# Kernel tuning notes

Hardware: AMD Instinct MI355X
Metric: run time of the kernel (lower is better)

The kernel has to match this reference:

```python
import jax, jax.numpy as jnp
import numpy as np

EPS = 1e-7  # keras backend epsilon

def setup_inputs() -> dict:
    key = jax.random.key(0)
    k1, k2, k3 = jax.random.split(key, 3)
    B, L, D, P = 16, 1024, 256, 20
    sent1 = jax.random.normal(k1, (B, L, D), dtype=jnp.float32)
    sent2 = jax.random.normal(k2, (B, L, D), dtype=jnp.float32)
    kernel = jax.random.normal(k3, (P, D), dtype=jnp.float32) * 0.1
    return {"sent1": sent1, "sent2": sent2, "kernel": kernel}

def reference(sent1, sent2, kernel):
    # token norms with keras-style clamping: sqrt(max(sum(x^2), eps))
    n1 = jnp.sqrt(jnp.maximum(jnp.sum(sent1 * sent1, axis=-1), EPS))  # [B,L1]
    n2 = jnp.sqrt(jnp.maximum(jnp.sum(sent2 * sent2, axis=-1), EPS))  # [B,L2]
    # all-pairs cosine matrix via matmul instead of broadcast-multiply-reduce
    dots = jnp.einsum('bld,bmd->blm', sent1, sent2)                    # [B,L1,L2]
    cos = dots / n1[:, :, None] / n2[:, None, :]
    # mean attentive vectors: cosine-weighted sum of sent2, normalized by row sum
    weighted = jnp.einsum('blm,bmd->bld', cos, sent2)                  # [B,L1,D]
    mav = weighted / (jnp.sum(cos, axis=-1, keepdims=True) + EPS)      # [B,L1,D]
    # perspective-weighted cosine between sent1*k and mav*k, fused without [B,L,P,D]
    k2 = kernel * kernel                                               # [P,D]
    num = jnp.einsum('bld,pd->blp', sent1 * mav, k2)                   # sum_d s1*mav*k^2
    nv1 = jnp.sqrt(jnp.maximum(jnp.einsum('bld,pd->blp', sent1 * sent1, k2), EPS))
    nv2 = jnp.sqrt(jnp.maximum(jnp.einsum('bld,pd->blp', mav * mav, k2), EPS))
    return num / nv1 / nv2                                             # [B,L1,P]
```

## Files before the change

kernel.cpp:

```cpp
#include <hip/hip_runtime.h>
#include <math.h>

#define EPS 1e-7f

constexpr int B = 16, L = 1024, D = 256, P = 20;
constexpr int LD = L * D;
constexpr int DD = D * D;

typedef __attribute__((ext_vector_type(8))) _Float16 f16x8;
typedef __attribute__((ext_vector_type(4))) float f32x4;


__device__ inline unsigned short f2h(float x) {
    _Float16 h = (_Float16)x;
    union { _Float16 h; unsigned short u; } c; c.h = h; return c.u;
}
__device__ inline float h2f(unsigned short u) {
    union { unsigned short u; _Float16 h; } c; c.u = u; return (float)c.h;
}

__global__ __launch_bounds__(256) void k_prep2(const float* __restrict__ s2,
                                               float* __restrict__ tp,
                                               unsigned short* __restrict__ CT) {
    __shared__ float tile[32][257];
    __shared__ float wiv[32];
    __shared__ float wsq[32];
    int tid = threadIdx.x;
    int b   = blockIdx.x >> 5, mt = blockIdx.x & 31;
    int m0  = mt * 32;
    {
        int r = tid >> 3, c0 = (tid & 7) * 32;
        const float* gp = s2 + (size_t)b * LD + (size_t)(m0 + r) * D + c0;
        float4 v[8];
#pragma unroll
        for (int q = 0; q < 8; ++q) v[q] = ((const float4*)gp)[q];
#pragma unroll
        for (int q = 0; q < 8; ++q) *(float4*)&tile[r][c0 + q * 4] = v[q];
    }
    __syncthreads();
    {
        int r = tid >> 3, seg = tid & 7;
        float s = 0.f;
#pragma unroll
        for (int k = 0; k < 32; ++k) { float v = tile[r][seg * 32 + k]; s += v * v; }
#pragma unroll
        for (int o = 4; o; o >>= 1) s += __shfl_down(s, o, 8);
        if (seg == 0) {
            float iv = 1.0f / sqrtf(fmaxf(s, EPS));
            wiv[r] = iv;
            wsq[r] = sqrtf(iv);
        }
    }
    __syncthreads();
    {
        int dc = tid;
        float tpart = 0.f;
        union { unsigned short us[32]; uint4 q[4]; } ph;
#pragma unroll
        for (int m = 0; m < 32; ++m) {
            float v = tile[m][dc];
            tpart += v * wiv[m];
            ph.us[m] = f2h(v * wsq[m]);
        }
        tp[(size_t)(mt * B + b) * D + dc] = tpart;
        size_t o = (size_t)b * LD + (size_t)dc * L + m0;
        *(uint4*)(CT + o)      = ph.q[0]; *(uint4*)(CT + o + 8)  = ph.q[1];
        *(uint4*)(CT + o + 16) = ph.q[2]; *(uint4*)(CT + o + 24) = ph.q[3];
    }
}

__global__ __launch_bounds__(256) void k_gram32(const unsigned short* __restrict__ CT,
                                                unsigned short* __restrict__ Gf) {
    __shared__ short smem[2 * 32 * 264];
    short* As = smem;
    short* Bs = smem + 32 * 264;
    int tid  = threadIdx.x;
    int b    = blockIdx.x >> 6;
    int ti   = (blockIdx.x >> 3) & 7;
    int tj   = blockIdx.x & 7;
    int wave = tid >> 6, lane = tid & 63;
    int lr   = lane & 15, lq = lane >> 4;
    int srow = tid >> 3, sseg = (tid & 7) * 32;

    f32x4 acc[2][2];
#pragma unroll
    for (int i = 0; i < 2; ++i)
#pragma unroll
        for (int j = 0; j < 2; ++j) acc[i][j] = (f32x4){0.f, 0.f, 0.f, 0.f};

#pragma unroll 1
    for (int kb = 0; kb < 4; ++kb) {
        int koff = kb * 256;
        __syncthreads();
        {
            const unsigned short* ga = CT + (size_t)b * LD + (size_t)(ti * 32 + srow) * L + koff + sseg;
            uint4 a0 = ((const uint4*)ga)[0], a1 = ((const uint4*)ga)[1];
            uint4 a2 = ((const uint4*)ga)[2], a3 = ((const uint4*)ga)[3];
            const unsigned short* gb = CT + (size_t)b * LD + (size_t)(tj * 32 + srow) * L + koff + sseg;
            uint4 b0 = ((const uint4*)gb)[0], b1 = ((const uint4*)gb)[1];
            uint4 b2 = ((const uint4*)gb)[2], b3 = ((const uint4*)gb)[3];
            short* la = &As[srow * 264 + sseg];
            ((uint4*)la)[0] = a0; ((uint4*)la)[1] = a1;
            ((uint4*)la)[2] = a2; ((uint4*)la)[3] = a3;
            short* lb = &Bs[srow * 264 + sseg];
            ((uint4*)lb)[0] = b0; ((uint4*)lb)[1] = b1;
            ((uint4*)lb)[2] = b2; ((uint4*)lb)[3] = b3;
        }
        __syncthreads();
#pragma unroll
        for (int kk = 0; kk < 2; ++kk) {
            int ks = wave * 2 + kk;
            f16x8 af[2], bf[2];
#pragma unroll
            for (int i = 0; i < 2; ++i)
                af[i] = *(const f16x8*)&As[(i * 16 + lr) * 264 + ks * 32 + lq * 8];
#pragma unroll
            for (int j = 0; j < 2; ++j)
                bf[j] = *(const f16x8*)&Bs[(j * 16 + lr) * 264 + ks * 32 + lq * 8];
#pragma unroll
            for (int i = 0; i < 2; ++i)
#pragma unroll
                for (int j = 0; j < 2; ++j)
                    acc[i][j] = __builtin_amdgcn_mfma_f32_16x16x32_f16(af[i], bf[j], acc[i][j], 0, 0, 0);
        }
    }
    __syncthreads();
    float* red = (float*)smem;
#pragma unroll
    for (int i = 0; i < 2; ++i)
#pragma unroll
        for (int j = 0; j < 2; ++j)
#pragma unroll
            for (int r = 0; r < 4; ++r) {
                int row = i * 16 + lq * 4 + r, col = j * 16 + lr;
                red[wave * 1056 + row * 33 + col] = acc[i][j][r];
            }
    __syncthreads();
#pragma unroll
    for (int k = 0; k < 4; ++k) {
        int e = tid + k * 256;
        int row = e >> 5, col = e & 31;
        float s = red[row * 33 + col] + red[1056 + row * 33 + col] +
                  red[2112 + row * 33 + col] + red[3168 + row * 33 + col];
        Gf[(size_t)b * DD + (size_t)(ti * 32 + row) * D + tj * 32 + col] = f2h(s);
    }
}

__global__ __launch_bounds__(512) void k_mav_out(const float* __restrict__ s1,
                                                 const float* __restrict__ tp,
                                                 const unsigned short* __restrict__ Gf,
                                                 const float* __restrict__ kern,
                                                 float* __restrict__ out) {
    __shared__ short As[32 * 264];
    __shared__ short Bs[64 * 264];
    __shared__ short Ms[32 * 264];
    __shared__ float ts[D];
    __shared__ float sgnS[32];
    int tid  = threadIdx.x;
    int b    = blockIdx.x >> 5, lt = blockIdx.x & 31;
    int l0   = lt * 32;
    int wave = tid >> 6, lane = tid & 63;
    int lr   = lane & 15, lq = lane >> 4;

    if (tid < 256) {
        float a = 0.f;
#pragma unroll
        for (int mc = 0; mc < 32; ++mc) a += tp[(size_t)(mc * B + b) * D + tid];
        ts[tid] = a;
    }
    __syncthreads();

    {
        int r = tid >> 4, seg = tid & 15;
        const float* gp = s1 + (size_t)(b * L + l0 + r) * D + seg * 16;
        float up = 0.f, sq = 0.f;
        union { unsigned short us[16]; uint4 q[2]; } hb;
#pragma unroll
        for (int q4 = 0; q4 < 4; ++q4) {
            float4 v = ((const float4*)gp)[q4];
            int td = seg * 16 + q4 * 4;
            up += v.x * ts[td] + v.y * ts[td + 1] + v.z * ts[td + 2] + v.w * ts[td + 3];
            sq += v.x * v.x + v.y * v.y + v.z * v.z + v.w * v.w;
            hb.us[q4 * 4 + 0] = f2h(v.x); hb.us[q4 * 4 + 1] = f2h(v.y);
            hb.us[q4 * 4 + 2] = f2h(v.z); hb.us[q4 * 4 + 3] = f2h(v.w);
        }
        short* la = &As[r * 264 + seg * 16];
        ((uint4*)la)[0] = hb.q[0]; ((uint4*)la)[1] = hb.q[1];
#pragma unroll
        for (int o = 8; o; o >>= 1) { up += __shfl_down(up, o, 16); sq += __shfl_down(sq, o, 16); }
        if (seg == 0) {
            float n1v = sqrtf(fmaxf(sq, EPS));
            sgnS[r] = up + EPS * n1v;
        }
    }

    int wlr = (wave >> 2) * 16;
    int wnc = (wave & 3) * 16;
#pragma unroll 1
    for (int nh = 0; nh < 4; ++nh) {
        __syncthreads();
        {
            int r = tid >> 3, seg = (tid & 7) * 32;
            const unsigned short* gb = Gf + (size_t)b * DD + (size_t)(nh * 64 + r) * D + seg;
            uint4 b0 = ((const uint4*)gb)[0], b1 = ((const uint4*)gb)[1];
            uint4 b2 = ((const uint4*)gb)[2], b3 = ((const uint4*)gb)[3];
            short* lb = &Bs[r * 264 + seg];
            ((uint4*)lb)[0] = b0; ((uint4*)lb)[1] = b1;
            ((uint4*)lb)[2] = b2; ((uint4*)lb)[3] = b3;
        }
        __syncthreads();
        f32x4 acc = (f32x4){0.f, 0.f, 0.f, 0.f};
#pragma unroll
        for (int ks = 0; ks < 8; ++ks) {
            f16x8 af = *(const f16x8*)&As[(wlr + lr) * 264 + ks * 32 + lq * 8];
            f16x8 bf = *(const f16x8*)&Bs[(wnc + lr) * 264 + ks * 32 + lq * 8];
            acc = __builtin_amdgcn_mfma_f32_16x16x32_f16(af, bf, acc, 0, 0, 0);
        }
#pragma unroll
        for (int r4 = 0; r4 < 4; ++r4)
            Ms[(wlr + lq * 4 + r4) * 264 + nh * 64 + wnc + lr] = f2h(acc[r4]);
    }
    __syncthreads();

    float* k2s = (float*)Bs;
    {
        int d = tid & 255, ph = tid >> 8;
#pragma unroll
        for (int i = 0; i < 10; ++i) {
            int p = i * 2 + ph;
            float v = kern[p * D + d];
            k2s[p * 264 + d] = v * v;
        }
    }
    __syncthreads();

    int dg = lane & 15, ps = lane >> 4;
#pragma unroll 1
    for (int rl = 0; rl < 4; ++rl) {
        int l = wave * 4 + rl;
        float4 sm[4], ss[4], mm[4];
#pragma unroll
        for (int j = 0; j < 4; ++j) {
            ushort4 h4 = *(const ushort4*)&As[l * 264 + dg * 4 + j * 64];
            ushort4 m4 = *(const ushort4*)&Ms[l * 264 + dg * 4 + j * 64];
            float4 sv, mv;
            sv.x = h2f(h4.x); sv.y = h2f(h4.y); sv.z = h2f(h4.z); sv.w = h2f(h4.w);
            mv.x = h2f(m4.x); mv.y = h2f(m4.y); mv.z = h2f(m4.z); mv.w = h2f(m4.w);
            sm[j].x = sv.x * mv.x; sm[j].y = sv.y * mv.y; sm[j].z = sv.z * mv.z; sm[j].w = sv.w * mv.w;
            ss[j].x = sv.x * sv.x; ss[j].y = sv.y * sv.y; ss[j].z = sv.z * sv.z; ss[j].w = sv.w * sv.w;
            mm[j].x = mv.x * mv.x; mm[j].y = mv.y * mv.y; mm[j].z = mv.z * mv.z; mm[j].w = mv.w * mv.w;
        }
        float sgn = (sgnS[l] < 0.f) ? -1.f : 1.f;
#pragma unroll
        for (int tI = 0; tI < 5; ++tI) {
            int p = ps + tI * 4;
            float na = 0.f, nb = 0.f, nc = 0.f;
#pragma unroll
            for (int j = 0; j < 4; ++j) {
                float4 kv = *(const float4*)&k2s[p * 264 + j * 64 + dg * 4];
                na += sm[j].x * kv.x + sm[j].y * kv.y + sm[j].z * kv.z + sm[j].w * kv.w;
                nb += ss[j].x * kv.x + ss[j].y * kv.y + ss[j].z * kv.z + ss[j].w * kv.w;
                nc += mm[j].x * kv.x + mm[j].y * kv.y + mm[j].z * kv.z + mm[j].w * kv.w;
            }
#pragma unroll
            for (int o = 8; o; o >>= 1) {
                na += __shfl_down(na, o, 16);
                nb += __shfl_down(nb, o, 16);
                nc += __shfl_down(nc, o, 16);
            }
            if (dg == 0) {
                out[(size_t)(b * L + l0 + l) * P + p] =
                    sgn * na * rsqrtf(fmaxf(nb, EPS)) * rsqrtf(fmaxf(nc, EPS));
            }
        }
    }
}

extern "C" void kernel_launch(void* const* d_in, const int* in_sizes, int n_in,
                              void* d_out, int out_size, void* d_ws, size_t ws_size,
                              hipStream_t stream) {
    const float* s1   = (const float*)d_in[0];
    const float* s2   = (const float*)d_in[1];
    const float* kern = (const float*)d_in[2];
    float* out = (float*)d_out;
    float* ws  = (float*)d_ws;

    float* tp = ws;
    unsigned short* CT = (unsigned short*)(ws + 131072);
    unsigned short* Gf = (unsigned short*)(ws + 2228224);

    k_prep2<<<512, 256, 0, stream>>>(s2, tp, CT);
    k_gram32<<<1024, 256, 0, stream>>>(CT, Gf);
    k_mav_out<<<512, 512, 0, stream>>>(s1, tp, Gf, kern, out);
}
```

Baseline: 126.3 us.

## Load MFMA operands directly from global memory and widen prep kernel to 512 threads

The gram kernel no longer stages CT tiles through LDS. Each wave streams its own K-slice of f16 fragments straight from global memory into MFMA, which removes the per-iteration barriers and LDS copies. The mav kernel likewise reads Gf fragments directly from global memory, keeps its A fragments in registers, and computes the squared kernel up front alongside the ts reduction. The prep kernel doubles its thread count and splits the M dimension across two halves, combining the partial sums through shared memory. This trades LDS reuse for uncoalesced, per-lane 16-byte global loads that depend on cache hits.

Result: slower. 134.1 us (+6.2%).

```diff
diff --git a/kernel.cpp b/kernel.cpp
--- a/kernel.cpp
+++ b/kernel.cpp
@@ -19,32 +19,33 @@
     union { unsigned short u; _Float16 h; } c; c.u = u; return (float)c.h;
 }
 
-__global__ __launch_bounds__(256) void k_prep2(const float* __restrict__ s2,
+__global__ __launch_bounds__(512) void k_prep2(const float* __restrict__ s2,
                                                float* __restrict__ tp,
                                                unsigned short* __restrict__ CT) {
     __shared__ float tile[32][257];
     __shared__ float wiv[32];
     __shared__ float wsq[32];
+    __shared__ float tpp[2][256];
     int tid = threadIdx.x;
     int b   = blockIdx.x >> 5, mt = blockIdx.x & 31;
     int m0  = mt * 32;
     {
-        int r = tid >> 3, c0 = (tid & 7) * 32;
+        int r = tid >> 4, c0 = (tid & 15) * 16;
         const float* gp = s2 + (size_t)b * LD + (size_t)(m0 + r) * D + c0;
-        float4 v[8];
-#pragma unroll
-        for (int q = 0; q < 8; ++q) v[q] = ((const float4*)gp)[q];
-#pragma unroll
-        for (int q = 0; q < 8; ++q) *(float4*)&tile[r][c0 + q * 4] = v[q];
-    }
-    __syncthreads();
-    {
-        int r = tid >> 3, seg = tid & 7;
+        float4 v[4];
+#pragma unroll
+        for (int q = 0; q < 4; ++q) v[q] = ((const float4*)gp)[q];
+#pragma unroll
+        for (int q = 0; q < 4; ++q) *(float4*)&tile[r][c0 + q * 4] = v[q];
+    }
+    __syncthreads();
+    {
+        int r = tid >> 4, seg = tid & 15;
         float s = 0.f;
 #pragma unroll
-        for (int k = 0; k < 32; ++k) { float v = tile[r][seg * 32 + k]; s += v * v; }
-#pragma unroll
-        for (int o = 4; o; o >>= 1) s += __shfl_down(s, o, 8);
+        for (int k = 0; k < 16; ++k) { float v = tile[r][seg * 16 + k]; s += v * v; }
+#pragma unroll
+        for (int o = 8; o; o >>= 1) s += __shfl_down(s, o, 16);
         if (seg == 0) {
             float iv = 1.0f / sqrtf(fmaxf(s, EPS));
             wiv[r] = iv;
@@ -53,34 +54,37 @@
     }
     __syncthreads();
     {
-        int dc = tid;
+        int dc = tid & 255, h = tid >> 8;
         float tpart = 0.f;
-        union { unsigned short us[32]; uint4 q[4]; } ph;
-#pragma unroll
-        for (int m = 0; m < 32; ++m) {
+        union { unsigned short us[16]; uint4 q[2]; } ph;
+#pragma unroll
+        for (int mm = 0; mm < 16; ++mm) {
+            int m = h * 16 + mm;
             float v = tile[m][dc];
             tpart += v * wiv[m];
-            ph.us[m] = f2h(v * wsq[m]);
-        }
-        tp[(size_t)(mt * B + b) * D + dc] = tpart;
-        size_t o = (size_t)b * LD + (size_t)dc * L + m0;
-        *(uint4*)(CT + o)      = ph.q[0]; *(uint4*)(CT + o + 8)  = ph.q[1];
-        *(uint4*)(CT + o + 16) = ph.q[2]; *(uint4*)(CT + o + 24) = ph.q[3];
-    }
+            ph.us[mm] = f2h(v * wsq[m]);
+        }
+        tpp[h][dc] = tpart;
+        size_t o = (size_t)b * LD + (size_t)dc * L + m0 + h * 16;
+        *(uint4*)(CT + o) = ph.q[0]; *(uint4*)(CT + o + 8) = ph.q[1];
+    }
+    __syncthreads();
+    if (tid < 256)
+        tp[(size_t)(mt * B + b) * D + tid] = tpp[0][tid] + tpp[1][tid];
 }
 
 __global__ __launch_bounds__(256) void k_gram32(const unsigned short* __restrict__ CT,
                                                 unsigned short* __restrict__ Gf) {
-    __shared__ short smem[2 * 32 * 264];
-    short* As = smem;
-    short* Bs = smem + 32 * 264;
+    __shared__ float red[4 * 32 * 33];
     int tid  = threadIdx.x;
     int b    = blockIdx.x >> 6;
     int ti   = (blockIdx.x >> 3) & 7;
     int tj   = blockIdx.x & 7;
     int wave = tid >> 6, lane = tid & 63;
     int lr   = lane & 15, lq = lane >> 4;
-    int srow = tid >> 3, sseg = (tid & 7) * 32;
+
+    const unsigned short* baseA = CT + (size_t)b * LD + (size_t)(ti * 32 + lr) * L;
+    const unsigned short* baseB = CT + (size_t)b * LD + (size_t)(tj * 32 + lr) * L;
 
     f32x4 acc[2][2];
 #pragma unroll
@@ -88,44 +92,21 @@
 #pragma unroll
         for (int j = 0; j < 2; ++j) acc[i][j] = (f32x4){0.f, 0.f, 0.f, 0.f};
 
-#pragma unroll 1
-    for (int kb = 0; kb < 4; ++kb) {
-        int koff = kb * 256;
-        __syncthreads();
-        {
-            const unsigned short* ga = CT + (size_t)b * LD + (size_t)(ti * 32 + srow) * L + koff + sseg;
-            uint4 a0 = ((const uint4*)ga)[0], a1 = ((const uint4*)ga)[1];
-            uint4 a2 = ((const uint4*)ga)[2], a3 = ((const uint4*)ga)[3];
-            const unsigned short* gb = CT + (size_t)b * LD + (size_t)(tj * 32 + srow) * L + koff + sseg;
-            uint4 b0 = ((const uint4*)gb)[0], b1 = ((const uint4*)gb)[1];
-            uint4 b2 = ((const uint4*)gb)[2], b3 = ((const uint4*)gb)[3];
-            short* la = &As[srow * 264 + sseg];
-            ((uint4*)la)[0] = a0; ((uint4*)la)[1] = a1;
-            ((uint4*)la)[2] = a2; ((uint4*)la)[3] = a3;
-            short* lb = &Bs[srow * 264 + sseg];
-            ((uint4*)lb)[0] = b0; ((uint4*)lb)[1] = b1;
-            ((uint4*)lb)[2] = b2; ((uint4*)lb)[3] = b3;
-        }
-        __syncthreads();
-#pragma unroll
-        for (int kk = 0; kk < 2; ++kk) {
-            int ks = wave * 2 + kk;
-            f16x8 af[2], bf[2];
-#pragma unroll
-            for (int i = 0; i < 2; ++i)
-                af[i] = *(const f16x8*)&As[(i * 16 + lr) * 264 + ks * 32 + lq * 8];
+    int k0 = wave * 256 + lq * 8;
+#pragma unroll 4
+    for (int ks = 0; ks < 8; ++ks) {
+        int ko = k0 + ks * 32;
+        f16x8 af[2], bf[2];
+        af[0] = *(const f16x8*)(baseA + ko);
+        af[1] = *(const f16x8*)(baseA + 16 * L + ko);
+        bf[0] = *(const f16x8*)(baseB + ko);
+        bf[1] = *(const f16x8*)(baseB + 16 * L + ko);
+#pragma unroll
+        for (int i = 0; i < 2; ++i)
 #pragma unroll
             for (int j = 0; j < 2; ++j)
-                bf[j] = *(const f16x8*)&Bs[(j * 16 + lr) * 264 + ks * 32 + lq * 8];
-#pragma unroll
-            for (int i = 0; i < 2; ++i)
-#pragma unroll
-                for (int j = 0; j < 2; ++j)
-                    acc[i][j] = __builtin_amdgcn_mfma_f32_16x16x32_f16(af[i], bf[j], acc[i][j], 0, 0, 0);
-        }
-    }
-    __syncthreads();
-    float* red = (float*)smem;
+                acc[i][j] = __builtin_amdgcn_mfma_f32_16x16x32_f16(af[i], bf[j], acc[i][j], 0, 0, 0);
+    }
 #pragma unroll
     for (int i = 0; i < 2; ++i)
 #pragma unroll
@@ -152,8 +133,8 @@
                                                  const float* __restrict__ kern,
                                                  float* __restrict__ out) {
     __shared__ short As[32 * 264];
-    __shared__ short Bs[64 * 264];
     __shared__ short Ms[32 * 264];
+    __shared__ float k2s[P * 264];
     __shared__ float ts[D];
     __shared__ float sgnS[32];
     int tid  = threadIdx.x;
@@ -168,6 +149,15 @@
         for (int mc = 0; mc < 32; ++mc) a += tp[(size_t)(mc * B + b) * D + tid];
         ts[tid] = a;
     }
+    {
+        int d = tid & 255, ph = tid >> 8;
+#pragma unroll
+        for (int i = 0; i < 10; ++i) {
+            int p = i * 2 + ph;
+            float v = kern[p * D + d];
+            k2s[p * 264 + d] = v * v;
+        }
+    }
     __syncthreads();
 
     {
@@ -193,43 +183,28 @@
             sgnS[r] = up + EPS * n1v;
         }
     }
-
-    int wlr = (wave >> 2) * 16;
-    int wnc = (wave & 3) * 16;
+    __syncthreads();
+
+    {
+        int wlr = (wave >> 2) * 16;
+        int wnc = (wave & 3) * 16;
+        f16x8 af[8];
+#pragma unroll
+        for (int ks = 0; ks < 8; ++ks)
+            af[ks] = *(const f16x8*)&As[(wlr + lr) * 264 + ks * 32 + lq * 8];
+        const unsigned short* gb0 = Gf + (size_t)b * DD + (size_t)(wnc + lr) * D + lq * 8;
 #pragma unroll 1
-    for (int nh = 0; nh < 4; ++nh) {
-        __syncthreads();
-        {
-            int r = tid >> 3, seg = (tid & 7) * 32;
-            const unsigned short* gb = Gf + (size_t)b * DD + (size_t)(nh * 64 + r) * D + seg;
-            uint4 b0 = ((const uint4*)gb)[0], b1 = ((const uint4*)gb)[1];
-            uint4 b2 = ((const uint4*)gb)[2], b3 = ((const uint4*)gb)[3];
-            short* lb = &Bs[r * 264 + seg];
-            ((uint4*)lb)[0] = b0; ((uint4*)lb)[1] = b1;
-            ((uint4*)lb)[2] = b2; ((uint4*)lb)[3] = b3;
-        }
-        __syncthreads();
-        f32x4 acc = (f32x4){0.f, 0.f, 0.f, 0.f};
-#pragma unroll
-        for (int ks = 0; ks < 8; ++ks) {
-            f16x8 af = *(const f16x8*)&As[(wlr + lr) * 264 + ks * 32 + lq * 8];
-            f16x8 bf = *(const f16x8*)&Bs[(wnc + lr) * 264 + ks * 32 + lq * 8];
-            acc = __builtin_amdgcn_mfma_f32_16x16x32_f16(af, bf, acc, 0, 0, 0);
-        }
-#pragma unroll
-        for (int r4 = 0; r4 < 4; ++r4)
-            Ms[(wlr + lq * 4 + r4) * 264 + nh * 64 + wnc + lr] = f2h(acc[r4]);
-    }
-    __syncthreads();
-
-    float* k2s = (float*)Bs;
-    {
-        int d = tid & 255, ph = tid >> 8;
-#pragma unroll
-        for (int i = 0; i < 10; ++i) {
-            int p = i * 2 + ph;
-            float v = kern[p * D + d];
-            k2s[p * 264 + d] = v * v;
+        for (int nh = 0; nh < 4; ++nh) {
+            const unsigned short* gb = gb0 + (size_t)(nh * 64) * D;
+            f32x4 acc = (f32x4){0.f, 0.f, 0.f, 0.f};
+#pragma unroll
+            for (int ks = 0; ks < 8; ++ks) {
+                f16x8 bf = *(const f16x8*)(gb + ks * 32);
+                acc = __builtin_amdgcn_mfma_f32_16x16x32_f16(af[ks], bf, acc, 0, 0, 0);
+            }
+#pragma unroll
+            for (int r4 = 0; r4 < 4; ++r4)
+                Ms[(wlr + lq * 4 + r4) * 264 + nh * 64 + wnc + lr] = f2h(acc[r4]);
         }
     }
     __syncthreads();
@@ -289,7 +264,7 @@
     unsigned short* CT = (unsigned short*)(ws + 131072);
     unsigned short* Gf = (unsigned short*)(ws + 2228224);
 
-    k_prep2<<<512, 256, 0, stream>>>(s2, tp, CT);
+    k_prep2<<<512, 512, 0, stream>>>(s2, tp, CT);
     k_gram32<<<1024, 256, 0, stream>>>(CT, Gf);
     k_mav_out<<<512, 512, 0, stream>>>(s1, tp, Gf, kern, out);
 }
```
